# Kernel tuning notes

Measured on AMD Instinct MI355X. Metric: run time of the kernel, lower is better.

## Reference

```python
import jax, jax.numpy as jnp
import numpy as np

B, LQ, LV = 32, 64, 128
QS, FS, BN = 512, 1024, 512

def setup_inputs() -> dict:
    key = jax.random.key(0)
    k1, k2, k3, k4, k5 = jax.random.split(key, 5)
    s = lambda n: 1.0 / np.sqrt(n)
    return {
        "phr_feats": jax.random.normal(k1, (B, LQ, QS), dtype=jnp.float32),
        "vis_feats": jax.random.normal(k2, (B, LV, FS), dtype=jnp.float32),
        "W": jax.random.uniform(k3, (BN, QS), jnp.float32, -s(QS), s(QS)),
        "U": jax.random.uniform(k4, (BN, FS), jnp.float32, -s(FS), s(FS)),
        "b": jnp.ones((BN,), dtype=jnp.float32),
        "w": jax.random.uniform(k5, (1, BN), jnp.float32, -s(BN), s(BN)),
    }

def reference(phr_feats, vis_feats, W, U, b, w):
    # Wh: [B,Lq,BN], Uv: [B,Lv,BN]
    Wh = jnp.einsum('bqd,nd->bqn', phr_feats, W)
    Uv = jnp.einsum('bvf,nf->bvn', vis_feats, U)
    # broadcast add + tanh: [B,Lq,Lv,BN]
    t = jnp.tanh(Wh[:, :, None, :] + Uv[:, None, :, :] + b)
    energies = jnp.einsum('bqvn,n->bqv', t, w[0])  # squeeze(-1)
    weights = jax.nn.softmax(energies, axis=2)
    aligned = jnp.einsum('bqv,bvf->bqf', weights, vis_feats)
    semantic_group_feats = jnp.concatenate([phr_feats, aligned], axis=2)
    return (semantic_group_feats, weights, energies)
```

## Files before the change

### kernel.cpp

```cpp
#include <hip/hip_runtime.h>

#define NB  32
#define NLQ 64
#define NLV 128
#define NQS 512
#define NFS 1024
#define NBN 512
#define CC  2.8853900817779268f

typedef float  floatx4 __attribute__((ext_vector_type(4)));
typedef __bf16 bf16x8  __attribute__((ext_vector_type(8)));
typedef unsigned short us;
typedef __attribute__((address_space(1))) const unsigned int gu32;
typedef __attribute__((address_space(3))) unsigned int lu32;

__device__ __forceinline__ us f2bf(float f) {
    unsigned int u = __float_as_uint(f);
    u += 0x7fffu + ((u >> 16) & 1u);
    return (us)(u >> 16);
}
__device__ __forceinline__ unsigned int pktrunc(float lo, float hi) {
    return __builtin_amdgcn_perm(__float_as_uint(hi), __float_as_uint(lo), 0x07060302u);
}
__device__ __forceinline__ float blo(unsigned int u) {
    return __uint_as_float(u << 16);
}
__device__ __forceinline__ float bhi(unsigned int u) {
    return __uint_as_float(u & 0xffff0000u);
}

#define PHR4 262144
#define VIS4 1048576
#define WW4  65536
#define UU4  131072
#define TOT4 (PHR4 + VIS4 + WW4 + UU4)

__global__ __launch_bounds__(256) void convert_bf16(
    const float* __restrict__ phr, const float* __restrict__ vis,
    const float* __restrict__ W,   const float* __restrict__ U,
    us* __restrict__ phr_b, us* __restrict__ vis_b,
    us* __restrict__ W_b,   us* __restrict__ U_b,
    float* __restrict__ out_sgf)
{
    int i = blockIdx.x * 256 + threadIdx.x;
    if (i >= TOT4) return;
    const float* src; us* dst; int o;
    if (i < PHR4)              { src = phr; dst = phr_b; o = i; }
    else if (i < PHR4 + VIS4)  { src = vis; dst = vis_b; o = i - PHR4; }
    else if (i < PHR4 + VIS4 + WW4) { src = W; dst = W_b; o = i - PHR4 - VIS4; }
    else                       { src = U; dst = U_b; o = i - PHR4 - VIS4 - WW4; }
    float4 v = ((const float4*)src)[o];
    uint2 r = { pktrunc(v.x, v.y), pktrunc(v.z, v.w) };
    *(uint2*)(dst + (size_t)o * 4) = r;
    if (i < PHR4) {
        int row = o >> 7, c4 = o & 127;
        ((float4*)out_sgf)[(size_t)row * 384 + c4] = v;
    }
}

__device__ __forceinline__ void gemm64(
    us* smem,
    const us* __restrict__ A, const us* __restrict__ Bt,
    const float* __restrict__ bias,
    float* __restrict__ whYp, us* __restrict__ uvYTp,
    int K, int bx, int by)
{
    const int tid  = threadIdx.x;
    const int m0   = bx * 64;
    const int n0   = by * 64;
    const int wave = tid >> 6;
    const int lane = tid & 63;
    const int wm   = (wave >> 1) * 32;
    const int wn   = (wave & 1) * 32;
    const int fm   = lane & 15;
    const int c16  = lane >> 4;

    const int r0 = tid >> 3;
    const int lc = (tid & 7) ^ (r0 & 7);
    const us* ga0 = A  + (size_t)(m0 + r0)      * K + lc * 8;
    const us* ga1 = A  + (size_t)(m0 + r0 + 32) * K + lc * 8;
    const us* gb0 = Bt + (size_t)(n0 + r0)      * K + lc * 8;
    const us* gb1 = Bt + (size_t)(n0 + r0 + 32) * K + lc * 8;
    const int dst0 = wave * 512;
    const int dst1 = 2048 + wave * 512;

    floatx4 acc[2][2] = {};
    const int nt = K >> 6;

#define STAGE(bufbase, k0) do {                                                \
    us* as_ = (bufbase);  us* bs_ = (bufbase) + 4096;                          \
    __builtin_amdgcn_global_load_lds((gu32*)(ga0 + (k0)), (lu32*)(as_ + dst0), 16, 0, 0); \
    __builtin_amdgcn_global_load_lds((gu32*)(ga1 + (k0)), (lu32*)(as_ + dst1), 16, 0, 0); \
    __builtin_amdgcn_global_load_lds((gu32*)(gb0 + (k0)), (lu32*)(bs_ + dst0), 16, 0, 0); \
    __builtin_amdgcn_global_load_lds((gu32*)(gb1 + (k0)), (lu32*)(bs_ + dst1), 16, 0, 0); \
} while (0)

    STAGE(smem, 0);
    STAGE(smem + 8192, 64);
    int rs = 0;
    for (int t = 0; t < nt; ++t) {
        us* As = smem + rs * 8192;
        us* Bs = As + 4096;
        __builtin_amdgcn_s_barrier();
        __builtin_amdgcn_sched_barrier(0);
        if (t + 2 < nt) {
            int ss = rs + 2; if (ss >= 3) ss -= 3;
            STAGE(smem + ss * 8192, (t + 2) * 64);
            asm volatile("s_waitcnt vmcnt(8)" ::: "memory");
        } else if (t + 1 < nt) {
            asm volatile("s_waitcnt vmcnt(4)" ::: "memory");
        } else {
            asm volatile("s_waitcnt vmcnt(0)" ::: "memory");
        }
        __builtin_amdgcn_s_barrier();
        __builtin_amdgcn_sched_barrier(0);
        __builtin_amdgcn_s_setprio(1);
        #pragma unroll
        for (int ks = 0; ks < 2; ++ks) {
            bf16x8 am[2], bn[2];
            #pragma unroll
            for (int i = 0; i < 2; ++i) {
                int r  = wm + 16 * i + fm;
                int pc = (ks * 4 + c16) ^ (r & 7);
                am[i] = *(const bf16x8*)(As + r * 64 + pc * 8);
            }
            #pragma unroll
            for (int j = 0; j < 2; ++j) {
                int r  = wn + 16 * j + fm;
                int pc = (ks * 4 + c16) ^ (r & 7);
                bn[j] = *(const bf16x8*)(Bs + r * 64 + pc * 8);
            }
            #pragma unroll
            for (int i = 0; i < 2; ++i)
                #pragma unroll
                for (int j = 0; j < 2; ++j)
                    acc[i][j] = __builtin_amdgcn_mfma_f32_16x16x32_bf16(am[i], bn[j], acc[i][j], 0, 0, 0);
        }
        __builtin_amdgcn_s_setprio(0);
        rs = (rs == 2) ? 0 : rs + 1;
    }
#undef STAGE

    const int cr = (lane >> 4) * 4;
    const int cc = lane & 15;
    if (whYp) {
        #pragma unroll
        for (int j = 0; j < 2; ++j) {
            int gn = n0 + wn + 16 * j + cc;
            float bj = bias[gn];
            #pragma unroll
            for (int i = 0; i < 2; ++i)
                #pragma unroll
                for (int r = 0; r < 4; ++r) {
                    int gm = m0 + wm + 16 * i + cr + r;
                    whYp[(size_t)gm * NBN + gn] =
                        __builtin_amdgcn_exp2f(CC * (acc[i][j][r] + bj));
                }
        }
    } else {
        us* Cs = smem;
        __syncthreads();
        #pragma unroll
        for (int i = 0; i < 2; ++i)
            #pragma unroll
            for (int j = 0; j < 2; ++j) {
                int nl = wn + 16 * j + cc;
                int vl = wm + 16 * i + cr;
                #pragma unroll
                for (int r = 0; r < 4; ++r)
                    Cs[nl * 72 + vl + r] =
                        f2bf(__builtin_amdgcn_exp2f(CC * acc[i][j][r]));
            }
        __syncthreads();
        const int bb    = m0 >> 7;
        const int vbase = m0 & 127;
        const int nl    = tid >> 2;
        const int vc    = (tid & 3) * 16;
        uint4 t0 = *(const uint4*)(Cs + nl * 72 + vc);
        uint4 t1 = *(const uint4*)(Cs + nl * 72 + vc + 8);
        us* dst = uvYTp + ((size_t)bb * NBN + n0 + nl) * NLV + vbase + vc;
        *(uint4*)dst       = t0;
        *(uint4*)(dst + 8) = t1;
    }
}

__global__ __launch_bounds__(256) void gemm_both(
    const us* __restrict__ phr_b, const us* __restrict__ W_b,
    const float* __restrict__ bias,
    const us* __restrict__ vis_b, const us* __restrict__ U_b,
    float* __restrict__ whY, us* __restrict__ uvYT)
{
    __shared__ __align__(16) us smem[24576];
    int blk = blockIdx.x;
    if (blk < 256) {
        int bx = blk % 32, by = blk / 32;
        gemm64(smem, phr_b, W_b, bias, whY, nullptr, NQS, bx, by);
    } else {
        blk -= 256;
        int bx = blk % 64, by = blk / 64;
        gemm64(smem, vis_b, U_b, bias, nullptr, uvYT, NFS, bx, by);
    }
}

__global__ __launch_bounds__(512) void energize(
    const float* __restrict__ whY,
    const us* __restrict__ uvYT,
    const float* __restrict__ wvec,
    float* __restrict__ out_w, float* __restrict__ out_e,
    us* __restrict__ p_bf, us* __restrict__ p_lo)
{
    const float LOG2E = 1.4426950408889634f;
    int blk = blockIdx.x;
    blk = (blk & 7) * 64 + (blk >> 3);
    const int b    = blk >> 4;
    const int qq4  = blk & 15;
    const int tid  = threadIdx.x;
    const int wave = __builtin_amdgcn_readfirstlane(tid >> 6);
    const int lane = tid & 63;
    const int q0   = qq4 * 4;

    __shared__ float part[4][8][NLV];

    float4 sw0 = *(const float4*)(wvec + lane * 8);
    float4 sw1 = *(const float4*)(wvec + lane * 8 + 4);
    float sumw = sw0.x + sw0.y + sw0.z + sw0.w + sw1.x + sw1.y + sw1.z + sw1.w;
    #pragma unroll
    for (int off = 32; off; off >>= 1) sumw += __shfl_xor(sumw, off);

    const float* yqp = whY + (size_t)(b * NLQ + q0) * NBN + wave * 64;
    const float* wp  = wvec + wave * 64;
    const us*    uvp = uvYT + ((size_t)b * NBN + wave * 64) * NLV + 2 * lane;

    float acc[4][2] = {};
    #pragma unroll 2
    for (int nc = 0; nc < 64; nc += 8) {
        unsigned int yv[8];
        #pragma unroll
        for (int k = 0; k < 8; ++k)
            yv[k] = *(const unsigned int*)(uvp + (size_t)(nc + k) * NLV);
        #pragma unroll
        for (int kk = 0; kk < 4; ++kk) {
            const int k0 = nc + 2 * kk, k1 = k0 + 1;
            float x0a = blo(yv[2 * kk]),     x0b = bhi(yv[2 * kk]);
            float x1a = blo(yv[2 * kk + 1]), x1b = bhi(yv[2 * kk + 1]);
            float w0 = wp[k0], w1 = wp[k1];
            #pragma unroll
            for (int q = 0; q < 4; ++q) {
                float y0 = yqp[q * NBN + k0];
                float y1 = yqp[q * NBN + k1];
                float d0a = fmaf(x0a, y0, 1.f), d1a = fmaf(x1a, y1, 1.f);
                float d0b = fmaf(x0b, y0, 1.f), d1b = fmaf(x1b, y1, 1.f);
                float numa = fmaf(w0, d1a, w1 * d0a);
                float numb = fmaf(w0, d1b, w1 * d0b);
                acc[q][0] = fmaf(numa, __builtin_amdgcn_rcpf(d0a * d1a), acc[q][0]);
                acc[q][1] = fmaf(numb, __builtin_amdgcn_rcpf(d0b * d1b), acc[q][1]);
            }
        }
    }
    #pragma unroll
    for (int q = 0; q < 4; ++q) {
        float2 t = { acc[q][0], acc[q][1] };
        *(float2*)&part[q][wave][2 * lane] = t;
    }
    __syncthreads();

    if (wave < 4) {
        const int q = wave;
        float s0 = 0.f, s1 = 0.f;
        #pragma unroll
        for (int nq = 0; nq < 8; ++nq) {
            s0 += part[q][nq][2 * lane];
            s1 += part[q][nq][2 * lane + 1];
        }
        float e0 = sumw - 2.f * s0;
        float e1 = sumw - 2.f * s1;
        float m = fmaxf(e0, e1);
        #pragma unroll
        for (int off = 32; off; off >>= 1) m = fmaxf(m, __shfl_xor(m, off));
        float x0 = __builtin_amdgcn_exp2f((e0 - m) * LOG2E);
        float x1 = __builtin_amdgcn_exp2f((e1 - m) * LOG2E);
        float ss = x0 + x1;
        #pragma unroll
        for (int off = 32; off; off >>= 1) ss += __shfl_xor(ss, off);
        float inv = __builtin_amdgcn_rcpf(ss);
        float p0 = x0 * inv, p1 = x1 * inv;

        const size_t row = (size_t)(b * NLQ + q0 + q);
        float2 ep = { e0, e1 };
        float2 pp = { p0, p1 };
        *(float2*)(out_e + row * NLV + 2 * lane) = ep;
        *(float2*)(out_w + row * NLV + 2 * lane) = pp;
        unsigned int pb0 = f2bf(p0), pb1 = f2bf(p1);
        float lo0 = p0 - __uint_as_float(pb0 << 16);
        float lo1 = p1 - __uint_as_float(pb1 << 16);
        unsigned int lb0 = f2bf(lo0), lb1 = f2bf(lo1);
        *(unsigned int*)(p_bf + row * NLV + 2 * lane) = pb0 | (pb1 << 16);
        *(unsigned int*)(p_lo + row * NLV + 2 * lane) = lb0 | (lb1 << 16);
    }
}

__global__ __launch_bounds__(256) void aligned_mfma(
    const us* __restrict__ p_bf, const us* __restrict__ p_lo,
    const us* __restrict__ vis_b,
    float* __restrict__ out_sgf)
{
    int blk = blockIdx.x;
    blk = (blk & 7) * 64 + (blk >> 3);
    const int b    = blk >> 4;
    const int ft   = blk & 15;
    const int tid  = threadIdx.x;
    const int wave = tid >> 6;
    const int lane = tid & 63;
    const int wm   = (wave >> 1) * 32;
    const int wf   = (wave & 1) * 32;
    const int fm   = lane & 15;
    const int fko  = (lane >> 4) * 8;

    __shared__ us Vs[64][136];

    {
        const int v  = tid >> 1;
        const int fh = (tid & 1) * 32;
        const us* vp = vis_b + ((size_t)b * NLV + v) * NFS + ft * 64 + fh;
        #pragma unroll
        for (int r = 0; r < 8; ++r) {
            uint2 u = *(const uint2*)(vp + 4 * r);
            Vs[fh + 4 * r + 0][v] = (us)(u.x & 0xffffu);
            Vs[fh + 4 * r + 1][v] = (us)(u.x >> 16);
            Vs[fh + 4 * r + 2][v] = (us)(u.y & 0xffffu);
            Vs[fh + 4 * r + 3][v] = (us)(u.y >> 16);
        }
    }
    __syncthreads();

    floatx4 acc[2][2] = {};
    const us* pA  = p_bf + ((size_t)b * NLQ + wm + fm) * NLV + fko;
    const us* pAl = p_lo + ((size_t)b * NLQ + wm + fm) * NLV + fko;

    #pragma unroll
    for (int ks = 0; ks < 4; ++ks) {
        bf16x8 a[2], al[2], bb2[2];
        #pragma unroll
        for (int i = 0; i < 2; ++i) {
            a[i]  = *(const bf16x8*)(pA  + (size_t)i * 16 * NLV + ks * 32);
            al[i] = *(const bf16x8*)(pAl + (size_t)i * 16 * NLV + ks * 32);
        }
        #pragma unroll
        for (int j = 0; j < 2; ++j)
            bb2[j] = *(const bf16x8*)&Vs[wf + 16 * j + fm][ks * 32 + fko];
        #pragma unroll
        for (int i = 0; i < 2; ++i)
            #pragma unroll
            for (int j = 0; j < 2; ++j) {
                acc[i][j] = __builtin_amdgcn_mfma_f32_16x16x32_bf16(a[i],  bb2[j], acc[i][j], 0, 0, 0);
                acc[i][j] = __builtin_amdgcn_mfma_f32_16x16x32_bf16(al[i], bb2[j], acc[i][j], 0, 0, 0);
            }
    }

    const int cr = (lane >> 4) * 4;
    const int cc = lane & 15;
    #pragma unroll
    for (int i = 0; i < 2; ++i)
        #pragma unroll
        for (int j = 0; j < 2; ++j)
            #pragma unroll
            for (int r = 0; r < 4; ++r) {
                int q = wm + 16 * i + cr + r;
                int f = ft * 64 + wf + 16 * j + cc;
                size_t row = (size_t)b * NLQ + q;
                out_sgf[row * (NQS + NFS) + NQS + f] = acc[i][j][r];
            }
}

extern "C" void kernel_launch(void* const* d_in, const int* in_sizes, int n_in,
                              void* d_out, int out_size, void* d_ws, size_t ws_size,
                              hipStream_t stream) {
    const float* phr  = (const float*)d_in[0];
    const float* vis  = (const float*)d_in[1];
    const float* W    = (const float*)d_in[2];
    const float* U    = (const float*)d_in[3];
    const float* bias = (const float*)d_in[4];
    const float* wvec = (const float*)d_in[5];

    char* ws = (char*)d_ws;
    us* phr_b   = (us*)ws;
    us* vis_b   = (us*)(ws + (2u << 20));
    us* W_b     = (us*)(ws + (10u << 20));
    us* U_b     = (us*)(ws + (10u << 20) + (512u << 10));
    float* whY  = (float*)(ws + (12u << 20));
    us* uvYT    = (us*)(ws + (16u << 20));
    us* p_bf    = (us*)(ws + (20u << 20));
    us* p_lo    = (us*)(ws + (20u << 20) + (512u << 10));

    float* out     = (float*)d_out;
    float* out_sgf = out;
    float* out_w   = out_sgf + (size_t)NB * NLQ * (NQS + NFS);
    float* out_e   = out_w   + (size_t)NB * NLQ * NLV;

    convert_bf16<<<TOT4 / 256, 256, 0, stream>>>(
        phr, vis, W, U, phr_b, vis_b, W_b, U_b, out_sgf);
    gemm_both<<<768, 256, 0, stream>>>(phr_b, W_b, bias, vis_b, U_b, whY, uvYT);
    energize<<<512, 512, 0, stream>>>(whY, uvYT, wvec, out_w, out_e, p_bf, p_lo);
    aligned_mfma<<<512, 256, 0, stream>>>(p_bf, p_lo, vis_b, out_sgf);
}
```

Baseline: 117.6 us.

## Fuse aligned-feature matmul into energize kernel using LDS-held softmax weights

```diff
diff --git a/kernel.cpp b/kernel.cpp
--- a/kernel.cpp
+++ b/kernel.cpp
@@ -202,12 +202,13 @@
     }
 }
 
-__global__ __launch_bounds__(512) void energize(
+__global__ __launch_bounds__(512) void attn2(
     const float* __restrict__ whY,
     const us* __restrict__ uvYT,
     const float* __restrict__ wvec,
-    float* __restrict__ out_w, float* __restrict__ out_e,
-    us* __restrict__ p_bf, us* __restrict__ p_lo)
+    const us* __restrict__ vis_b,
+    float* __restrict__ out_sgf, float* __restrict__ out_w,
+    float* __restrict__ out_e)
 {
     const float LOG2E = 1.4426950408889634f;
     int blk = blockIdx.x;
@@ -220,6 +221,7 @@
     const int q0   = qq4 * 4;
 
     __shared__ float part[4][8][NLV];
+    __shared__ float p_s[4][NLV];
 
     float4 sw0 = *(const float4*)(wvec + lane * 8);
     float4 sw1 = *(const float4*)(wvec + lane * 8 + 4);
@@ -290,86 +292,36 @@
         float2 pp = { p0, p1 };
         *(float2*)(out_e + row * NLV + 2 * lane) = ep;
         *(float2*)(out_w + row * NLV + 2 * lane) = pp;
-        unsigned int pb0 = f2bf(p0), pb1 = f2bf(p1);
-        float lo0 = p0 - __uint_as_float(pb0 << 16);
-        float lo1 = p1 - __uint_as_float(pb1 << 16);
-        unsigned int lb0 = f2bf(lo0), lb1 = f2bf(lo1);
-        *(unsigned int*)(p_bf + row * NLV + 2 * lane) = pb0 | (pb1 << 16);
-        *(unsigned int*)(p_lo + row * NLV + 2 * lane) = lb0 | (lb1 << 16);
-    }
-}
-
-__global__ __launch_bounds__(256) void aligned_mfma(
-    const us* __restrict__ p_bf, const us* __restrict__ p_lo,
-    const us* __restrict__ vis_b,
-    float* __restrict__ out_sgf)
-{
-    int blk = blockIdx.x;
-    blk = (blk & 7) * 64 + (blk >> 3);
-    const int b    = blk >> 4;
-    const int ft   = blk & 15;
-    const int tid  = threadIdx.x;
-    const int wave = tid >> 6;
-    const int lane = tid & 63;
-    const int wm   = (wave >> 1) * 32;
-    const int wf   = (wave & 1) * 32;
-    const int fm   = lane & 15;
-    const int fko  = (lane >> 4) * 8;
-
-    __shared__ us Vs[64][136];
-
-    {
-        const int v  = tid >> 1;
-        const int fh = (tid & 1) * 32;
-        const us* vp = vis_b + ((size_t)b * NLV + v) * NFS + ft * 64 + fh;
-        #pragma unroll
-        for (int r = 0; r < 8; ++r) {
-            uint2 u = *(const uint2*)(vp + 4 * r);
-            Vs[fh + 4 * r + 0][v] = (us)(u.x & 0xffffu);
-            Vs[fh + 4 * r + 1][v] = (us)(u.x >> 16);
-            Vs[fh + 4 * r + 2][v] = (us)(u.y & 0xffffu);
-            Vs[fh + 4 * r + 3][v] = (us)(u.y >> 16);
-        }
+        p_s[q][2 * lane]     = p0;
+        p_s[q][2 * lane + 1] = p1;
     }
     __syncthreads();
 
-    floatx4 acc[2][2] = {};
-    const us* pA  = p_bf + ((size_t)b * NLQ + wm + fm) * NLV + fko;
-    const us* pAl = p_lo + ((size_t)b * NLQ + wm + fm) * NLV + fko;
-
+    const int f0 = tid << 1;
+    float2 acc2[4] = {};
+    const us* vb = vis_b + (size_t)b * NLV * NFS + f0;
+    for (int v0 = 0; v0 < NLV; v0 += 4) {
+        float4 pv[4];
+        #pragma unroll
+        for (int qq = 0; qq < 4; ++qq) pv[qq] = *(const float4*)&p_s[qq][v0];
+        #pragma unroll
+        for (int dv = 0; dv < 4; ++dv) {
+            unsigned int u = *(const unsigned int*)(vb + (size_t)(v0 + dv) * NFS);
+            float x0 = blo(u), x1 = bhi(u);
+            #pragma unroll
+            for (int qq = 0; qq < 4; ++qq) {
+                float p = (dv == 0) ? pv[qq].x : (dv == 1) ? pv[qq].y
+                        : (dv == 2) ? pv[qq].z : pv[qq].w;
+                acc2[qq].x = fmaf(p, x0, acc2[qq].x);
+                acc2[qq].y = fmaf(p, x1, acc2[qq].y);
+            }
+        }
+    }
     #pragma unroll
-    for (int ks = 0; ks < 4; ++ks) {
-        bf16x8 a[2], al[2], bb2[2];
-        #pragma unroll
-        for (int i = 0; i < 2; ++i) {
-            a[i]  = *(const bf16x8*)(pA  + (size_t)i * 16 * NLV + ks * 32);
-            al[i] = *(const bf16x8*)(pAl + (size_t)i * 16 * NLV + ks * 32);
-        }
-        #pragma unroll
-        for (int j = 0; j < 2; ++j)
-            bb2[j] = *(const bf16x8*)&Vs[wf + 16 * j + fm][ks * 32 + fko];
-        #pragma unroll
-        for (int i = 0; i < 2; ++i)
-            #pragma unroll
-            for (int j = 0; j < 2; ++j) {
-                acc[i][j] = __builtin_amdgcn_mfma_f32_16x16x32_bf16(a[i],  bb2[j], acc[i][j], 0, 0, 0);
-                acc[i][j] = __builtin_amdgcn_mfma_f32_16x16x32_bf16(al[i], bb2[j], acc[i][j], 0, 0, 0);
-            }
-    }
-
-    const int cr = (lane >> 4) * 4;
-    const int cc = lane & 15;
-    #pragma unroll
-    for (int i = 0; i < 2; ++i)
-        #pragma unroll
-        for (int j = 0; j < 2; ++j)
-            #pragma unroll
-            for (int r = 0; r < 4; ++r) {
-                int q = wm + 16 * i + cr + r;
-                int f = ft * 64 + wf + 16 * j + cc;
-                size_t row = (size_t)b * NLQ + q;
-                out_sgf[row * (NQS + NFS) + NQS + f] = acc[i][j][r];
-            }
+    for (int qq = 0; qq < 4; ++qq) {
+        size_t row = (size_t)(b * NLQ + q0 + qq);
+        *(float2*)(out_sgf + row * (NQS + NFS) + NQS + f0) = acc2[qq];
+    }
 }
 
 extern "C" void kernel_launch(void* const* d_in, const int* in_sizes, int n_in,
@@ -389,8 +341,6 @@
     us* U_b     = (us*)(ws + (10u << 20) + (512u << 10));
     float* whY  = (float*)(ws + (12u << 20));
     us* uvYT    = (us*)(ws + (16u << 20));
-    us* p_bf    = (us*)(ws + (20u << 20));
-    us* p_lo    = (us*)(ws + (20u << 20) + (512u << 10));
 
     float* out     = (float*)d_out;
     float* out_sgf = out;
@@ -400,6 +350,6 @@
     convert_bf16<<<TOT4 / 256, 256, 0, stream>>>(
         phr, vis, W, U, phr_b, vis_b, W_b, U_b, out_sgf);
     gemm_both<<<768, 256, 0, stream>>>(phr_b, W_b, bias, vis_b, U_b, whY, uvYT);
-    energize<<<512, 512, 0, stream>>>(whY, uvYT, wvec, out_w, out_e, p_bf, p_lo);
-    aligned_mfma<<<512, 256, 0, stream>>>(p_bf, p_lo, vis_b, out_sgf);
-}
+    attn2<<<512, 512, 0, stream>>>(whY, uvYT, wvec, vis_b,
+                                   out_sgf, out_w, out_e);
+}
```

Result: slower. 120.2 us (+2.2%).
